# Kernel tuning notes

Hardware: AMD Instinct MI355X
Metric: run time of the kernel (lower is better)

The kernel has to match this reference:

```python
import jax, jax.numpy as jnp
import numpy as np

C = 256  # channels
B, H, W = 16, 64, 64


def _conv1x1(x, w, b):
    # x: [B,Cin,H,W], w: [Cout,Cin], b: [Cout] -> [B,Cout,H,W]
    return jnp.einsum('bchw,oc->bohw', x, w) + b[None, :, None, None]


def _axis_attn(x, wq, bq, wf, bf, axis):
    # axis: -1 for 'W', -2 for 'H'
    qkv = _conv1x1(x, wq, bq)                      # [B,1+2C,H,W]
    query = qkv[:, :1]                             # [B,1,H,W]
    key = qkv[:, 1:1 + C]                          # [B,C,H,W]
    value = qkv[:, 1 + C:]                         # [B,C,H,W]
    scores = jax.nn.softmax(query, axis=axis)      # softmax over spatial axis
    context = jnp.sum(key * scores, axis=axis, keepdims=True)  # [B,C,H,1] or [B,C,1,W]
    gate = jax.nn.sigmoid(value)
    out = x + gate * context                       # broadcast over reduced axis
    return _conv1x1(out, wf, bf)


def setup_inputs() -> dict:
    key = jax.random.key(0)
    ks = jax.random.split(key, 5)
    s_qkv = 1.0 / np.sqrt(C)
    s_fus = 1.0 / np.sqrt(C)
    return {
        'x': jax.random.normal(ks[0], (B, C, H, W), dtype=jnp.float32),
        'qkvW_w': jax.random.normal(ks[1], (1 + 2 * C, C), dtype=jnp.float32) * s_qkv,
        'qkvW_b': jnp.zeros((1 + 2 * C,), dtype=jnp.float32),
        'qkvH_w': jax.random.normal(ks[2], (1 + 2 * C, C), dtype=jnp.float32) * s_qkv,
        'qkvH_b': jnp.zeros((1 + 2 * C,), dtype=jnp.float32),
        'fusW_w': jax.random.normal(ks[3], (C, C), dtype=jnp.float32) * s_fus,
        'fusW_b': jnp.zeros((C,), dtype=jnp.float32),
        'fusH_w': jax.random.normal(ks[4], (C, C), dtype=jnp.float32) * s_fus,
        'fusH_b': jnp.zeros((C,), dtype=jnp.float32),
    }


def reference(x, qkvW_w, qkvW_b, qkvH_w, qkvH_b, fusW_w, fusW_b, fusH_w, fusH_b):
    x_w = _axis_attn(x, qkvW_w, qkvW_b, fusW_w, fusW_b, axis=-1)
    x_h = _axis_attn(x_w, qkvH_w, qkvH_b, fusH_w, fusH_b, axis=-2)
    return x_h
```

## Files before the change

kernel.cpp:

```cpp
#include <hip/hip_runtime.h>

typedef unsigned short u16;
typedef unsigned int u32;
typedef __attribute__((ext_vector_type(8))) short bf16x8;
typedef __attribute__((ext_vector_type(4))) float f32x4;

__device__ __forceinline__ u16 f2bf(float f) {
    u32 u = __builtin_bit_cast(u32, f);
    u += 0x7FFFu + ((u >> 16) & 1u);
    return (u16)(u >> 16);
}
__device__ __forceinline__ float bf2f(u16 s) {
    u32 u = ((u32)s) << 16;
    return __builtin_bit_cast(float, u);
}
__device__ __forceinline__ float sigm(float x) {
    return 1.0f / (1.0f + __expf(-x));
}
__device__ __forceinline__ void gload16(const u16* g, u16* l) {
    __builtin_amdgcn_global_load_lds(
        (const __attribute__((address_space(1))) void*)g,
        (__attribute__((address_space(3))) void*)l, 16, 0, 0);
}

__global__ __launch_bounds__(256) void transpose_in(const float* __restrict__ x,
                                                    u16* __restrict__ xp) {
    __shared__ float tile[64][65];
    int bid = blockIdx.x;
    int ct = bid & 3, h = (bid >> 2) & 63, b = bid >> 8;
    int t = threadIdx.x;
    int tr = t >> 4, tc = t & 15;
    const float* src = x + (((size_t)(b * 256 + ct * 64) * 64 + h) * 64);
#pragma unroll
    for (int i = 0; i < 4; ++i) {
        int c = tr + i * 16;
        float4 v = *(const float4*)(src + (size_t)c * 4096 + tc * 4);
        tile[c][tc * 4 + 0] = v.x;
        tile[c][tc * 4 + 1] = v.y;
        tile[c][tc * 4 + 2] = v.z;
        tile[c][tc * 4 + 3] = v.w;
    }
    __syncthreads();
    u16* dst = xp + ((size_t)((b * 64 + h) * 64)) * 256 + ct * 64;
#pragma unroll
    for (int i = 0; i < 4; ++i) {
        int w = tr + i * 16;
        ushort4 o;
        o.x = f2bf(tile[tc * 4 + 0][w]);
        o.y = f2bf(tile[tc * 4 + 1][w]);
        o.z = f2bf(tile[tc * 4 + 2][w]);
        o.w = f2bf(tile[tc * 4 + 3][w]);
        *(ushort4*)(dst + (size_t)w * 256 + tc * 4) = o;
    }
}

__global__ __launch_bounds__(256) void prep_w(const float* __restrict__ qw,
                                              const float* __restrict__ qb,
                                              const float* __restrict__ fw,
                                              const float* __restrict__ fb,
                                              float* __restrict__ wq0,
                                              u16* __restrict__ wkv,
                                              float* __restrict__ bkv,
                                              u16* __restrict__ wf,
                                              float* __restrict__ bff) {
    int i = blockIdx.x * 256 + threadIdx.x;
    if (i < 513 * 256) {
        int o = i >> 8, c = i & 255;
        float v = qw[i];
        if (o == 0) wq0[c] = v;
        else        wkv[(size_t)(o - 1) * 256 + c] = f2bf(v);
    }
    if (i < 65536) wf[i] = f2bf(fw[i]);
    if (i < 512)   bkv[i] = qb[i + 1];
    if (i < 256)   bff[i] = fb[i];
}

template <int AXIS>
__global__ __launch_bounds__(256) void line_ctx(
    const u16* __restrict__ A, const u16* __restrict__ Wk,
    const float* __restrict__ wq0, const float* __restrict__ bkv,
    float* __restrict__ ctx) {
    __shared__ alignas(16) u16 Xl[64 * 256];
    __shared__ float ql[64];
    __shared__ float sc[64];
    __shared__ alignas(16) float ys[256];
    int t = threadIdx.x, lane = t & 63, wv = t >> 6;
    int l = blockIdx.x;
    auto prow = [&](int r) -> size_t {
        if (AXIS == 0) return (size_t)l * 64 + r;
        else           return (size_t)(l >> 6) * 4096 + (size_t)r * 64 + (l & 63);
    };
#pragma unroll
    for (int i = 0; i < 8; ++i) {
        int row = i * 8 + wv * 2 + (lane >> 5);
        int slot = (lane & 31) ^ (row & 7);
        gload16(A + prow(row) * 256 + slot * 8, &Xl[(i * 8 + wv * 2) * 256]);
    }
    __syncthreads();
    {
        int row = t >> 2, g = t & 3;
        const float* wp = wq0 + g * 64;
        float a = 0.f;
#pragma unroll
        for (int cc = 0; cc < 8; ++cc) {
            int slot = (g * 8 + cc) ^ (row & 7);
            bf16x8 v = *(const bf16x8*)&Xl[row * 256 + slot * 8];
#pragma unroll
            for (int j = 0; j < 8; ++j) a += bf2f((u16)v[j]) * wp[cc * 8 + j];
        }
        a += __shfl_xor(a, 1);
        a += __shfl_xor(a, 2);
        if (g == 0) ql[row] = a;
    }
    __syncthreads();
    if (t < 64) {
        float qv = ql[t];
        float m = qv;
#pragma unroll
        for (int off = 32; off > 0; off >>= 1) m = fmaxf(m, __shfl_xor(m, off));
        float e = __expf(qv - m);
        float s = e;
#pragma unroll
        for (int off = 32; off > 0; off >>= 1) s += __shfl_xor(s, off);
        sc[t] = e / s;
    }
    __syncthreads();
    {
        int chunk = t >> 3, e7 = t & 7;
        float a = 0.f;
#pragma unroll 8
        for (int p = 0; p < 64; ++p) {
            int slot = chunk ^ (p & 7);
            a += bf2f(Xl[p * 256 + slot * 8 + e7]) * sc[p];
        }
        ys[t] = a;
    }
    __syncthreads();
    {
        const u16* wk = Wk + (size_t)t * 256;
        float a = 0.f;
#pragma unroll
        for (int kc = 0; kc < 32; ++kc) {
            bf16x8 w = *(const bf16x8*)(wk + kc * 8);
#pragma unroll
            for (int j = 0; j < 8; ++j) a += bf2f((u16)w[j]) * ys[kc * 8 + j];
        }
        ctx[(size_t)l * 256 + t] = a + bkv[t];
    }
}

template <int AXIS>
__global__ __launch_bounds__(256, 2) void val_gate(
    const u16* __restrict__ A, const u16* __restrict__ Wv,
    const float* __restrict__ bv, const float* __restrict__ ctx,
    u16* __restrict__ G) {
    int h = blockIdx.x;
    int xcd = h & 7, slot = h >> 3;
    int otile = slot & 1, ptile = xcd * 64 + (slot >> 1);
    __shared__ alignas(16) u16 Asm[128 * 64];
    __shared__ alignas(16) u16 Bsm[128 * 64];
    int p0 = ptile * 128, o0 = otile * 128;
    int t = threadIdx.x, lane = t & 63, wv = t >> 6;
    int wm = (wv >> 1) * 64, wn = (wv & 1) * 64;
    int l7 = lane & 7;
    int srcoff = (lane >> 3) * 256 + (((lane & 7) ^ (lane >> 3)) * 8);
    int arow = lane & 15, kgrp = lane >> 4;
    f32x4 zero = {0.f, 0.f, 0.f, 0.f};
    f32x4 acc[4][4];
#pragma unroll
    for (int i = 0; i < 4; ++i)
#pragma unroll
        for (int jj = 0; jj < 4; ++jj) acc[i][jj] = zero;

    for (int k0 = 0; k0 < 256; k0 += 64) {
        __syncthreads();
#pragma unroll
        for (int it = 0; it < 4; ++it) {
            int r0 = it * 32 + wv * 8;
            gload16(A + (size_t)(p0 + r0) * 256 + k0 + srcoff, &Asm[r0 * 64]);
            gload16(Wv + (size_t)(o0 + r0) * 256 + k0 + srcoff, &Bsm[r0 * 64]);
        }
        __syncthreads();
#pragma unroll
        for (int kk = 0; kk < 64; kk += 32) {
            int soff = (((kk >> 3) + kgrp) ^ l7) << 3;
            bf16x8 af[4], bfv[4];
#pragma unroll
            for (int mi = 0; mi < 4; ++mi)
                af[mi] = *(const bf16x8*)&Asm[(wm + mi * 16 + arow) * 64 + soff];
#pragma unroll
            for (int ni = 0; ni < 4; ++ni)
                bfv[ni] = *(const bf16x8*)&Bsm[(wn + ni * 16 + arow) * 64 + soff];
#pragma unroll
            for (int mi = 0; mi < 4; ++mi)
#pragma unroll
                for (int ni = 0; ni < 4; ++ni)
                    acc[mi][ni] = __builtin_amdgcn_mfma_f32_16x16x32_bf16(
                        af[mi], bfv[ni], acc[mi][ni], 0, 0, 0);
        }
    }
#pragma unroll
    for (int mi = 0; mi < 4; ++mi) {
#pragma unroll
        for (int ni = 0; ni < 4; ++ni) {
            int col = o0 + wn + ni * 16 + arow;
            float bias = bv[col];
#pragma unroll
            for (int r = 0; r < 4; ++r) {
                int row = p0 + wm + mi * 16 + (kgrp << 2) + r;
                int line = (AXIS == 0) ? (row >> 6) : ((row >> 12) * 64 + (row & 63));
                float cx = ctx[(size_t)line * 256 + col];
                float xv = bf2f(A[(size_t)row * 256 + col]);
                float v = acc[mi][ni][r] + bias;
                G[(size_t)row * 256 + col] = f2bf(xv + sigm(v) * cx);
            }
        }
    }
}

template <int MODE>
__global__ __launch_bounds__(256, 2) void gemm_k(
    const u16* __restrict__ A, const u16* __restrict__ Bw,
    const float* __restrict__ bias,
    u16* __restrict__ bOut, float* __restrict__ fOut) {
    int h = blockIdx.x;
    int xcd = h & 7, slot = h >> 3;
    int otile = slot & 1, ptile = xcd * 64 + (slot >> 1);
    __shared__ alignas(16) u16 Asm[128 * 64];
    __shared__ alignas(16) u16 Bsm[128 * 64];
    int p0 = ptile * 128, o0 = otile * 128;
    int t = threadIdx.x, lane = t & 63, wv = t >> 6;
    int wm = (wv >> 1) * 64, wn = (wv & 1) * 64;
    int l7 = lane & 7;
    int srcoff = (lane >> 3) * 256 + (((lane & 7) ^ (lane >> 3)) * 8);
    int arow = lane & 15, kgrp = lane >> 4;
    f32x4 zero = {0.f, 0.f, 0.f, 0.f};
    f32x4 acc[4][4];
#pragma unroll
    for (int i = 0; i < 4; ++i)
#pragma unroll
        for (int jj = 0; jj < 4; ++jj) acc[i][jj] = zero;

    for (int k0 = 0; k0 < 256; k0 += 64) {
        __syncthreads();
#pragma unroll
        for (int it = 0; it < 4; ++it) {
            int r0 = it * 32 + wv * 8;
            gload16(A + (size_t)(p0 + r0) * 256 + k0 + srcoff, &Asm[r0 * 64]);
            gload16(Bw + (size_t)(o0 + r0) * 256 + k0 + srcoff, &Bsm[r0 * 64]);
        }
        __syncthreads();
#pragma unroll
        for (int kk = 0; kk < 64; kk += 32) {
            int soff = (((kk >> 3) + kgrp) ^ l7) << 3;
            bf16x8 af[4], bfv[4];
#pragma unroll
            for (int mi = 0; mi < 4; ++mi)
                af[mi] = *(const bf16x8*)&Asm[(wm + mi * 16 + arow) * 64 + soff];
#pragma unroll
            for (int ni = 0; ni < 4; ++ni)
                bfv[ni] = *(const bf16x8*)&Bsm[(wn + ni * 16 + arow) * 64 + soff];
#pragma unroll
            for (int mi = 0; mi < 4; ++mi)
#pragma unroll
                for (int ni = 0; ni < 4; ++ni)
                    acc[mi][ni] = __builtin_amdgcn_mfma_f32_16x16x32_bf16(
                        af[mi], bfv[ni], acc[mi][ni], 0, 0, 0);
        }
    }
#pragma unroll
    for (int mi = 0; mi < 4; ++mi) {
#pragma unroll
        for (int ni = 0; ni < 4; ++ni) {
            int col = o0 + wn + ni * 16 + arow;
            float bv = bias[col];
#pragma unroll
            for (int r = 0; r < 4; ++r) {
                int row = p0 + wm + mi * 16 + ((lane >> 4) << 2) + r;
                float v = acc[mi][ni][r] + bv;
                if (MODE == 1) {
                    bOut[(size_t)row * 256 + col] = f2bf(v);
                } else {
                    fOut[((size_t)((row >> 12) * 256 + col)) * 4096 + (row & 4095)] = v;
                }
            }
        }
    }
}

extern "C" void kernel_launch(void* const* d_in, const int* in_sizes, int n_in,
                              void* d_out, int out_size, void* d_ws, size_t ws_size,
                              hipStream_t stream) {
    const float* x   = (const float*)d_in[0];
    const float* qWw = (const float*)d_in[1];
    const float* qWb = (const float*)d_in[2];
    const float* qHw = (const float*)d_in[3];
    const float* qHb = (const float*)d_in[4];
    const float* fWw = (const float*)d_in[5];
    const float* fWb = (const float*)d_in[6];
    const float* fHw = (const float*)d_in[7];
    const float* fHb = (const float*)d_in[8];
    float* out = (float*)d_out;

    char* ws = (char*)d_ws;
    size_t off = 0;
    auto carve = [&](size_t bytes) -> void* {
        off = (off + 255) & ~(size_t)255;
        void* p = ws + off;
        off += bytes;
        return p;
    };
    const size_t P = 65536;
    u16*   xp  = (u16*)carve(P * 256 * 2);
    u16*   kb  = (u16*)carve(P * 256 * 2);
    u16*   vb  = (u16*)carve(P * 256 * 2);
    float* ctxb = (float*)carve(1024 * 256 * 4);
    float* wq01 = (float*)carve(256 * 4);
    u16*   wkv1 = (u16*)carve(512 * 256 * 2);
    float* bkv1 = (float*)carve(512 * 4);
    u16*   wf1  = (u16*)carve(65536 * 2);
    float* bf1  = (float*)carve(256 * 4);
    float* wq02 = (float*)carve(256 * 4);
    u16*   wkv2 = (u16*)carve(512 * 256 * 2);
    float* bkv2 = (float*)carve(512 * 4);
    u16*   wf2  = (u16*)carve(65536 * 2);
    float* bf2  = (float*)carve(256 * 4);

    prep_w<<<513, 256, 0, stream>>>(qWw, qWb, fWw, fWb, wq01, wkv1, bkv1, wf1, bf1);
    prep_w<<<513, 256, 0, stream>>>(qHw, qHb, fHw, fHb, wq02, wkv2, bkv2, wf2, bf2);
    transpose_in<<<4096, 256, 0, stream>>>(x, xp);

    line_ctx<0><<<1024, 256, 0, stream>>>(xp, wkv1, wq01, bkv1, ctxb);
    val_gate<0><<<1024, 256, 0, stream>>>(xp, wkv1 + 256 * 256, bkv1 + 256,
                                          ctxb, kb);
    gemm_k<1><<<1024, 256, 0, stream>>>(kb, wf1, bf1, vb, nullptr);
    line_ctx<1><<<1024, 256, 0, stream>>>(vb, wkv2, wq02, bkv2, ctxb);
    val_gate<1><<<1024, 256, 0, stream>>>(vb, wkv2 + 256 * 256, bkv2 + 256,
                                          ctxb, kb);
    gemm_k<2><<<1024, 256, 0, stream>>>(kb, wf2, bf2, nullptr, out);
    (void)in_sizes; (void)n_in; (void)out_size; (void)ws_size;
}
```

Before: 167.3 us.

## Vectorize GEMM epilogues via operand swap, LDS transpose, and shared ctx tiles

Measured after the change: 178.4 us. 6.6% more time.

```diff
diff --git a/kernel.cpp b/kernel.cpp
--- a/kernel.cpp
+++ b/kernel.cpp
@@ -159,12 +159,21 @@
     int otile = slot & 1, ptile = xcd * 64 + (slot >> 1);
     __shared__ alignas(16) u16 Asm[128 * 64];
     __shared__ alignas(16) u16 Bsm[128 * 64];
-    int p0 = ptile * 128, o0 = otile * 128;
+    __shared__ alignas(16) float ctxs[2][128];
+    int o0 = otile * 128;
     int t = threadIdx.x, lane = t & 63, wv = t >> 6;
-    int wm = (wv >> 1) * 64, wn = (wv & 1) * 64;
-    int l7 = lane & 7;
-    int srcoff = (lane >> 3) * 256 + (((lane & 7) ^ (lane >> 3)) * 8);
-    int arow = lane & 15, kgrp = lane >> 4;
+    int arow = lane & 15, kgrp = lane >> 4, l7 = lane & 7;
+    int rowhalf = wv & 1, chhalf = wv >> 1;
+    auto prow = [&](int r) -> size_t {
+        if (AXIS == 0) return (size_t)ptile * 128 + r;
+        else           return (size_t)(ptile >> 5) * 4096 + (size_t)(r & 63) * 64 +
+                              ((ptile & 31) * 2) + (r >> 6);
+    };
+    int lbase = (AXIS == 0) ? (ptile * 2) : ((ptile >> 5) * 64 + (ptile & 31) * 2);
+    {
+        int ll = t >> 7, cl = t & 127;
+        ctxs[ll][cl] = ctx[(size_t)(lbase + ll) * 256 + o0 + cl];
+    }
     f32x4 zero = {0.f, 0.f, 0.f, 0.f};
     f32x4 acc[4][4];
 #pragma unroll
@@ -177,43 +186,47 @@
 #pragma unroll
         for (int it = 0; it < 4; ++it) {
             int r0 = it * 32 + wv * 8;
-            gload16(A + (size_t)(p0 + r0) * 256 + k0 + srcoff, &Asm[r0 * 64]);
-            gload16(Wv + (size_t)(o0 + r0) * 256 + k0 + srcoff, &Bsm[r0 * 64]);
+            int rr = r0 + (lane >> 3);
+            int chs = ((l7 ^ (lane >> 3)) * 8);
+            gload16(A + prow(rr) * 256 + k0 + chs, &Asm[r0 * 64]);
+            gload16(Wv + (size_t)(o0 + rr) * 256 + k0 + chs, &Bsm[r0 * 64]);
         }
         __syncthreads();
 #pragma unroll
         for (int kk = 0; kk < 64; kk += 32) {
             int soff = (((kk >> 3) + kgrp) ^ l7) << 3;
-            bf16x8 af[4], bfv[4];
-#pragma unroll
-            for (int mi = 0; mi < 4; ++mi)
-                af[mi] = *(const bf16x8*)&Asm[(wm + mi * 16 + arow) * 64 + soff];
-#pragma unroll
-            for (int ni = 0; ni < 4; ++ni)
-                bfv[ni] = *(const bf16x8*)&Bsm[(wn + ni * 16 + arow) * 64 + soff];
-#pragma unroll
-            for (int mi = 0; mi < 4; ++mi)
-#pragma unroll
-                for (int ni = 0; ni < 4; ++ni)
-                    acc[mi][ni] = __builtin_amdgcn_mfma_f32_16x16x32_bf16(
-                        af[mi], bfv[ni], acc[mi][ni], 0, 0, 0);
-        }
-    }
-#pragma unroll
-    for (int mi = 0; mi < 4; ++mi) {
-#pragma unroll
-        for (int ni = 0; ni < 4; ++ni) {
-            int col = o0 + wn + ni * 16 + arow;
-            float bias = bv[col];
-#pragma unroll
-            for (int r = 0; r < 4; ++r) {
-                int row = p0 + wm + mi * 16 + (kgrp << 2) + r;
-                int line = (AXIS == 0) ? (row >> 6) : ((row >> 12) * 64 + (row & 63));
-                float cx = ctx[(size_t)line * 256 + col];
-                float xv = bf2f(A[(size_t)row * 256 + col]);
-                float v = acc[mi][ni][r] + bias;
-                G[(size_t)row * 256 + col] = f2bf(xv + sigm(v) * cx);
-            }
+            bf16x8 xf[4], wf[4];
+#pragma unroll
+            for (int xi = 0; xi < 4; ++xi)
+                xf[xi] = *(const bf16x8*)&Asm[(rowhalf * 64 + xi * 16 + arow) * 64 + soff];
+#pragma unroll
+            for (int wi = 0; wi < 4; ++wi)
+                wf[wi] = *(const bf16x8*)&Bsm[(chhalf * 64 + wi * 16 + arow) * 64 + soff];
+#pragma unroll
+            for (int wi = 0; wi < 4; ++wi)
+#pragma unroll
+                for (int xi = 0; xi < 4; ++xi)
+                    acc[wi][xi] = __builtin_amdgcn_mfma_f32_16x16x32_bf16(
+                        wf[wi], xf[xi], acc[wi][xi], 0, 0, 0);
+        }
+    }
+#pragma unroll
+    for (int wi = 0; wi < 4; ++wi) {
+        int chl = chhalf * 64 + wi * 16 + kgrp * 4;
+        int ch = o0 + chl;
+        f32x4 bq = *(const f32x4*)&bv[ch];
+        f32x4 cx = *(const f32x4*)&ctxs[rowhalf][chl];
+#pragma unroll
+        for (int xi = 0; xi < 4; ++xi) {
+            int row = rowhalf * 64 + xi * 16 + arow;
+            size_t p = prow(row);
+            ushort4 xv = *(const ushort4*)(A + p * 256 + ch);
+            ushort4 o;
+            o.x = f2bf(bf2f(xv.x) + sigm(acc[wi][xi][0] + bq[0]) * cx[0]);
+            o.y = f2bf(bf2f(xv.y) + sigm(acc[wi][xi][1] + bq[1]) * cx[1]);
+            o.z = f2bf(bf2f(xv.z) + sigm(acc[wi][xi][2] + bq[2]) * cx[2]);
+            o.w = f2bf(bf2f(xv.w) + sigm(acc[wi][xi][3] + bq[3]) * cx[3]);
+            *(ushort4*)(G + p * 256 + ch) = o;
         }
     }
 }
@@ -228,6 +241,7 @@
     int otile = slot & 1, ptile = xcd * 64 + (slot >> 1);
     __shared__ alignas(16) u16 Asm[128 * 64];
     __shared__ alignas(16) u16 Bsm[128 * 64];
+    __shared__ alignas(16) float tb[(MODE == 2) ? 64 * 132 : 4];
     int p0 = ptile * 128, o0 = otile * 128;
     int t = threadIdx.x, lane = t & 63, wv = t >> 6;
     int wm = (wv >> 1) * 64, wn = (wv & 1) * 64;
@@ -260,30 +274,69 @@
 #pragma unroll
             for (int ni = 0; ni < 4; ++ni)
                 bfv[ni] = *(const bf16x8*)&Bsm[(wn + ni * 16 + arow) * 64 + soff];
-#pragma unroll
-            for (int mi = 0; mi < 4; ++mi)
+            if (MODE == 1) {
 #pragma unroll
                 for (int ni = 0; ni < 4; ++ni)
-                    acc[mi][ni] = __builtin_amdgcn_mfma_f32_16x16x32_bf16(
-                        af[mi], bfv[ni], acc[mi][ni], 0, 0, 0);
-        }
-    }
-#pragma unroll
-    for (int mi = 0; mi < 4; ++mi) {
+#pragma unroll
+                    for (int mi = 0; mi < 4; ++mi)
+                        acc[ni][mi] = __builtin_amdgcn_mfma_f32_16x16x32_bf16(
+                            bfv[ni], af[mi], acc[ni][mi], 0, 0, 0);
+            } else {
+#pragma unroll
+                for (int mi = 0; mi < 4; ++mi)
+#pragma unroll
+                    for (int ni = 0; ni < 4; ++ni)
+                        acc[mi][ni] = __builtin_amdgcn_mfma_f32_16x16x32_bf16(
+                            af[mi], bfv[ni], acc[mi][ni], 0, 0, 0);
+            }
+        }
+    }
+    if (MODE == 1) {
 #pragma unroll
         for (int ni = 0; ni < 4; ++ni) {
-            int col = o0 + wn + ni * 16 + arow;
-            float bv = bias[col];
-#pragma unroll
-            for (int r = 0; r < 4; ++r) {
-                int row = p0 + wm + mi * 16 + ((lane >> 4) << 2) + r;
-                float v = acc[mi][ni][r] + bv;
-                if (MODE == 1) {
-                    bOut[(size_t)row * 256 + col] = f2bf(v);
-                } else {
-                    fOut[((size_t)((row >> 12) * 256 + col)) * 4096 + (row & 4095)] = v;
+            int col0 = o0 + wn + ni * 16 + kgrp * 4;
+            f32x4 bq = *(const f32x4*)&bias[col0];
+#pragma unroll
+            for (int mi = 0; mi < 4; ++mi) {
+                int row = p0 + wm + mi * 16 + arow;
+                ushort4 o;
+                o.x = f2bf(acc[ni][mi][0] + bq[0]);
+                o.y = f2bf(acc[ni][mi][1] + bq[1]);
+                o.z = f2bf(acc[ni][mi][2] + bq[2]);
+                o.w = f2bf(acc[ni][mi][3] + bq[3]);
+                *(ushort4*)(bOut + (size_t)row * 256 + col0) = o;
+            }
+        }
+    } else {
+        int bb = p0 >> 12, pl = p0 & 4095;
+#pragma unroll
+        for (int cp = 0; cp < 2; ++cp) {
+            if ((wv & 1) == cp) {
+#pragma unroll
+                for (int ni = 0; ni < 4; ++ni) {
+                    int c = ni * 16 + arow;
+                    float bvv = bias[o0 + cp * 64 + c];
+#pragma unroll
+                    for (int mi = 0; mi < 4; ++mi) {
+                        int r0w = wm + mi * 16 + kgrp * 4;
+                        f32x4 v;
+                        v[0] = acc[mi][ni][0] + bvv;
+                        v[1] = acc[mi][ni][1] + bvv;
+                        v[2] = acc[mi][ni][2] + bvv;
+                        v[3] = acc[mi][ni][3] + bvv;
+                        *(f32x4*)&tb[c * 132 + r0w] = v;
+                    }
                 }
             }
+            __syncthreads();
+#pragma unroll
+            for (int i = 0; i < 8; ++i) {
+                int c = i * 8 + (t >> 5);
+                f32x4 v = *(const f32x4*)&tb[c * 132 + (t & 31) * 4];
+                *(float4*)&fOut[(size_t)(bb * 256 + o0 + cp * 64 + c) * 4096 +
+                                pl + (t & 31) * 4] = *(float4*)&v;
+            }
+            if (cp == 0) __syncthreads();
         }
     }
 }
```

## Fuse value-gate GEMM with fusion GEMM keeping gated tile in LDS

Applied to the files above, without the earlier changes.

Result: slower. 189.8 us (+13.5%).

```diff
diff --git a/kernel.cpp b/kernel.cpp
--- a/kernel.cpp
+++ b/kernel.cpp
@@ -59,20 +59,25 @@
                                               const float* __restrict__ fw,
                                               const float* __restrict__ fb,
                                               float* __restrict__ wq0,
-                                              u16* __restrict__ wkv,
+                                              u16* __restrict__ wkvK,
+                                              u16* __restrict__ wkvV,
                                               float* __restrict__ bkv,
-                                              u16* __restrict__ wf,
+                                              u16* __restrict__ wfP,
                                               float* __restrict__ bff) {
     int i = blockIdx.x * 256 + threadIdx.x;
     if (i < 513 * 256) {
         int o = i >> 8, c = i & 255;
         float v = qw[i];
-        if (o == 0) wq0[c] = v;
-        else        wkv[(size_t)(o - 1) * 256 + c] = f2bf(v);
-    }
-    if (i < 65536) wf[i] = f2bf(fw[i]);
-    if (i < 512)   bkv[i] = qb[i + 1];
-    if (i < 256)   bff[i] = fb[i];
+        if (o == 0)        wq0[c] = v;
+        else if (o < 257)  wkvK[(size_t)(o - 1) * 256 + c] = f2bf(v);
+        else               wkvV[(c >> 3) * 2048 + (o - 257) * 8 + (c & 7)] = f2bf(v);
+    }
+    if (i < 65536) {
+        int o = i >> 8, c = i & 255;
+        wfP[(c >> 3) * 2048 + o * 8 + (c & 7)] = f2bf(fw[i]);
+    }
+    if (i < 512) bkv[i] = qb[i + 1];
+    if (i < 256) bff[i] = fb[i];
 }
 
 template <int AXIS>
@@ -149,140 +154,144 @@
     }
 }
 
-template <int AXIS>
-__global__ __launch_bounds__(256, 2) void val_gate(
-    const u16* __restrict__ A, const u16* __restrict__ Wv,
-    const float* __restrict__ bv, const float* __restrict__ ctx,
-    u16* __restrict__ G) {
-    int h = blockIdx.x;
-    int xcd = h & 7, slot = h >> 3;
-    int otile = slot & 1, ptile = xcd * 64 + (slot >> 1);
-    __shared__ alignas(16) u16 Asm[128 * 64];
-    __shared__ alignas(16) u16 Bsm[128 * 64];
-    int p0 = ptile * 128, o0 = otile * 128;
-    int t = threadIdx.x, lane = t & 63, wv = t >> 6;
-    int wm = (wv >> 1) * 64, wn = (wv & 1) * 64;
-    int l7 = lane & 7;
-    int srcoff = (lane >> 3) * 256 + (((lane & 7) ^ (lane >> 3)) * 8);
+template <int AXIS, int MODE>
+__global__ __launch_bounds__(512, 2) void fused_stage(
+    const u16* __restrict__ A, const u16* __restrict__ WvP,
+    const float* __restrict__ bv, const u16* __restrict__ WfP,
+    const float* __restrict__ bfb, const float* __restrict__ ctx,
+    u16* __restrict__ bOut, float* __restrict__ fOut) {
+    __shared__ alignas(16) u16 Xsm[128 * 256];
+    __shared__ alignas(16) u16 Wsm[1024 * 8];
+    int t = threadIdx.x, lane = t & 63;
+    int wv = t >> 6, rowhalf = wv >> 2, chslab = (wv & 3) * 64;
     int arow = lane & 15, kgrp = lane >> 4;
+    int p0 = blockIdx.x * 128;
+#pragma unroll
+    for (int i = 0; i < 8; ++i) {
+        int d = t + i * 512;
+        int row = d >> 5, chunk = d & 31;
+        gload16(A + (size_t)(p0 + row) * 256 + ((chunk ^ (row & 7)) * 8),
+                &Xsm[d * 8]);
+    }
     f32x4 zero = {0.f, 0.f, 0.f, 0.f};
     f32x4 acc[4][4];
 #pragma unroll
-    for (int i = 0; i < 4; ++i)
-#pragma unroll
-        for (int jj = 0; jj < 4; ++jj) acc[i][jj] = zero;
-
-    for (int k0 = 0; k0 < 256; k0 += 64) {
+    for (int a = 0; a < 4; ++a)
+#pragma unroll
+        for (int b = 0; b < 4; ++b) acc[a][b] = zero;
+    for (int k0 = 0; k0 < 256; k0 += 32) {
         __syncthreads();
-#pragma unroll
-        for (int it = 0; it < 4; ++it) {
-            int r0 = it * 32 + wv * 8;
-            gload16(A + (size_t)(p0 + r0) * 256 + k0 + srcoff, &Asm[r0 * 64]);
-            gload16(Wv + (size_t)(o0 + r0) * 256 + k0 + srcoff, &Bsm[r0 * 64]);
-        }
+        gload16(WvP + k0 * 256 + t * 8, &Wsm[t * 8]);
+        gload16(WvP + k0 * 256 + (t + 512) * 8, &Wsm[(t + 512) * 8]);
         __syncthreads();
-#pragma unroll
-        for (int kk = 0; kk < 64; kk += 32) {
-            int soff = (((kk >> 3) + kgrp) ^ l7) << 3;
-            bf16x8 af[4], bfv[4];
-#pragma unroll
-            for (int mi = 0; mi < 4; ++mi)
-                af[mi] = *(const bf16x8*)&Asm[(wm + mi * 16 + arow) * 64 + soff];
-#pragma unroll
-            for (int ni = 0; ni < 4; ++ni)
-                bfv[ni] = *(const bf16x8*)&Bsm[(wn + ni * 16 + arow) * 64 + soff];
-#pragma unroll
-            for (int mi = 0; mi < 4; ++mi)
-#pragma unroll
-                for (int ni = 0; ni < 4; ++ni)
-                    acc[mi][ni] = __builtin_amdgcn_mfma_f32_16x16x32_bf16(
-                        af[mi], bfv[ni], acc[mi][ni], 0, 0, 0);
-        }
-    }
-#pragma unroll
-    for (int mi = 0; mi < 4; ++mi) {
-#pragma unroll
-        for (int ni = 0; ni < 4; ++ni) {
-            int col = o0 + wn + ni * 16 + arow;
-            float bias = bv[col];
-#pragma unroll
-            for (int r = 0; r < 4; ++r) {
-                int row = p0 + wm + mi * 16 + (kgrp << 2) + r;
-                int line = (AXIS == 0) ? (row >> 6) : ((row >> 12) * 64 + (row & 63));
-                float cx = ctx[(size_t)line * 256 + col];
-                float xv = bf2f(A[(size_t)row * 256 + col]);
-                float v = acc[mi][ni][r] + bias;
-                G[(size_t)row * 256 + col] = f2bf(xv + sigm(v) * cx);
+        bf16x8 wf[4], xf[4];
+#pragma unroll
+        for (int wi = 0; wi < 4; ++wi)
+            wf[wi] = *(const bf16x8*)&Wsm[kgrp * 2048 + (chslab + wi * 16 + arow) * 8];
+#pragma unroll
+        for (int xi = 0; xi < 4; ++xi) {
+            int p = rowhalf * 64 + xi * 16 + arow;
+            xf[xi] = *(const bf16x8*)&Xsm[p * 256 + (((k0 >> 3) + kgrp) ^ (p & 7)) * 8];
+        }
+#pragma unroll
+        for (int wi = 0; wi < 4; ++wi)
+#pragma unroll
+            for (int xi = 0; xi < 4; ++xi)
+                acc[wi][xi] = __builtin_amdgcn_mfma_f32_16x16x32_bf16(
+                    wf[wi], xf[xi], acc[wi][xi], 0, 0, 0);
+    }
+    __syncthreads();
+#pragma unroll
+    for (int wi = 0; wi < 4; ++wi) {
+        int ch = chslab + wi * 16 + kgrp * 4;
+        f32x4 bq = *(const f32x4*)&bv[ch];
+        f32x4 cx0;
+        if (AXIS == 0)
+            cx0 = *(const f32x4*)&ctx[(size_t)((p0 >> 6) + rowhalf) * 256 + ch];
+#pragma unroll
+        for (int xi = 0; xi < 4; ++xi) {
+            int row = rowhalf * 64 + xi * 16 + arow;
+            f32x4 cx;
+            if (AXIS == 0) {
+                cx = cx0;
+            } else {
+                int pg = p0 + row;
+                int line = ((pg >> 12) << 6) + (pg & 63);
+                cx = *(const f32x4*)&ctx[(size_t)line * 256 + ch];
             }
-        }
-    }
-}
-
-template <int MODE>
-__global__ __launch_bounds__(256, 2) void gemm_k(
-    const u16* __restrict__ A, const u16* __restrict__ Bw,
-    const float* __restrict__ bias,
-    u16* __restrict__ bOut, float* __restrict__ fOut) {
-    int h = blockIdx.x;
-    int xcd = h & 7, slot = h >> 3;
-    int otile = slot & 1, ptile = xcd * 64 + (slot >> 1);
-    __shared__ alignas(16) u16 Asm[128 * 64];
-    __shared__ alignas(16) u16 Bsm[128 * 64];
-    int p0 = ptile * 128, o0 = otile * 128;
-    int t = threadIdx.x, lane = t & 63, wv = t >> 6;
-    int wm = (wv >> 1) * 64, wn = (wv & 1) * 64;
-    int l7 = lane & 7;
-    int srcoff = (lane >> 3) * 256 + (((lane & 7) ^ (lane >> 3)) * 8);
-    int arow = lane & 15, kgrp = lane >> 4;
-    f32x4 zero = {0.f, 0.f, 0.f, 0.f};
-    f32x4 acc[4][4];
-#pragma unroll
-    for (int i = 0; i < 4; ++i)
-#pragma unroll
-        for (int jj = 0; jj < 4; ++jj) acc[i][jj] = zero;
-
-    for (int k0 = 0; k0 < 256; k0 += 64) {
+            int idx = row * 256 + (((ch >> 3) ^ (row & 7)) * 8) + (ch & 7);
+            ushort4 xv = *(const ushort4*)&Xsm[idx];
+            ushort4 o;
+            o.x = f2bf(bf2f(xv.x) + sigm(acc[wi][xi][0] + bq[0]) * cx[0]);
+            o.y = f2bf(bf2f(xv.y) + sigm(acc[wi][xi][1] + bq[1]) * cx[1]);
+            o.z = f2bf(bf2f(xv.z) + sigm(acc[wi][xi][2] + bq[2]) * cx[2]);
+            o.w = f2bf(bf2f(xv.w) + sigm(acc[wi][xi][3] + bq[3]) * cx[3]);
+            *(ushort4*)&Xsm[idx] = o;
+        }
+    }
+#pragma unroll
+    for (int a = 0; a < 4; ++a)
+#pragma unroll
+        for (int b = 0; b < 4; ++b) acc[a][b] = zero;
+    for (int k0 = 0; k0 < 256; k0 += 32) {
         __syncthreads();
-#pragma unroll
-        for (int it = 0; it < 4; ++it) {
-            int r0 = it * 32 + wv * 8;
-            gload16(A + (size_t)(p0 + r0) * 256 + k0 + srcoff, &Asm[r0 * 64]);
-            gload16(Bw + (size_t)(o0 + r0) * 256 + k0 + srcoff, &Bsm[r0 * 64]);
-        }
+        gload16(WfP + k0 * 256 + t * 8, &Wsm[t * 8]);
+        gload16(WfP + k0 * 256 + (t + 512) * 8, &Wsm[(t + 512) * 8]);
         __syncthreads();
-#pragma unroll
-        for (int kk = 0; kk < 64; kk += 32) {
-            int soff = (((kk >> 3) + kgrp) ^ l7) << 3;
-            bf16x8 af[4], bfv[4];
-#pragma unroll
-            for (int mi = 0; mi < 4; ++mi)
-                af[mi] = *(const bf16x8*)&Asm[(wm + mi * 16 + arow) * 64 + soff];
-#pragma unroll
-            for (int ni = 0; ni < 4; ++ni)
-                bfv[ni] = *(const bf16x8*)&Bsm[(wn + ni * 16 + arow) * 64 + soff];
-#pragma unroll
-            for (int mi = 0; mi < 4; ++mi)
-#pragma unroll
-                for (int ni = 0; ni < 4; ++ni)
-                    acc[mi][ni] = __builtin_amdgcn_mfma_f32_16x16x32_bf16(
-                        af[mi], bfv[ni], acc[mi][ni], 0, 0, 0);
-        }
-    }
-#pragma unroll
-    for (int mi = 0; mi < 4; ++mi) {
-#pragma unroll
-        for (int ni = 0; ni < 4; ++ni) {
-            int col = o0 + wn + ni * 16 + arow;
-            float bv = bias[col];
-#pragma unroll
-            for (int r = 0; r < 4; ++r) {
-                int row = p0 + wm + mi * 16 + ((lane >> 4) << 2) + r;
-                float v = acc[mi][ni][r] + bv;
-                if (MODE == 1) {
-                    bOut[(size_t)row * 256 + col] = f2bf(v);
-                } else {
-                    fOut[((size_t)((row >> 12) * 256 + col)) * 4096 + (row & 4095)] = v;
-                }
+        bf16x8 wf[4], gf[4];
+#pragma unroll
+        for (int wi = 0; wi < 4; ++wi)
+            wf[wi] = *(const bf16x8*)&Wsm[kgrp * 2048 + (chslab + wi * 16 + arow) * 8];
+#pragma unroll
+        for (int xi = 0; xi < 4; ++xi) {
+            int p = rowhalf * 64 + xi * 16 + arow;
+            gf[xi] = *(const bf16x8*)&Xsm[p * 256 + (((k0 >> 3) + kgrp) ^ (p & 7)) * 8];
+        }
+        if (MODE == 1) {
+#pragma unroll
+            for (int wi = 0; wi < 4; ++wi)
+#pragma unroll
+                for (int xi = 0; xi < 4; ++xi)
+                    acc[wi][xi] = __builtin_amdgcn_mfma_f32_16x16x32_bf16(
+                        wf[wi], gf[xi], acc[wi][xi], 0, 0, 0);
+        } else {
+#pragma unroll
+            for (int xi = 0; xi < 4; ++xi)
+#pragma unroll
+                for (int wi = 0; wi < 4; ++wi)
+                    acc[xi][wi] = __builtin_amdgcn_mfma_f32_16x16x32_bf16(
+                        gf[xi], wf[wi], acc[xi][wi], 0, 0, 0);
+        }
+    }
+    if (MODE == 1) {
+#pragma unroll
+        for (int wi = 0; wi < 4; ++wi) {
+            int ch = chslab + wi * 16 + kgrp * 4;
+            f32x4 bq = *(const f32x4*)&bfb[ch];
+#pragma unroll
+            for (int xi = 0; xi < 4; ++xi) {
+                int row = rowhalf * 64 + xi * 16 + arow;
+                ushort4 o;
+                o.x = f2bf(acc[wi][xi][0] + bq[0]);
+                o.y = f2bf(acc[wi][xi][1] + bq[1]);
+                o.z = f2bf(acc[wi][xi][2] + bq[2]);
+                o.w = f2bf(acc[wi][xi][3] + bq[3]);
+                *(ushort4*)(bOut + (size_t)(p0 + row) * 256 + ch) = o;
+            }
+        }
+    } else {
+        int bb = p0 >> 12;
+#pragma unroll
+        for (int mi = 0; mi < 4; ++mi) {
+            int row0 = rowhalf * 64 + mi * 16 + kgrp * 4;
+#pragma unroll
+            for (int ni = 0; ni < 4; ++ni) {
+                int ch = chslab + ni * 16 + arow;
+                float bc = bfb[ch];
+                f32x4 v = acc[mi][ni];
+                v[0] += bc; v[1] += bc; v[2] += bc; v[3] += bc;
+                *(f32x4*)&fOut[((size_t)(bb * 256 + ch)) * 4096 +
+                               ((p0 + row0) & 4095)] = v;
             }
         }
     }
@@ -311,32 +320,33 @@
         return p;
     };
     const size_t P = 65536;
-    u16*   xp  = (u16*)carve(P * 256 * 2);
-    u16*   kb  = (u16*)carve(P * 256 * 2);
-    u16*   vb  = (u16*)carve(P * 256 * 2);
+    u16*   xp   = (u16*)carve(P * 256 * 2);
+    u16*   vb   = (u16*)carve(P * 256 * 2);
     float* ctxb = (float*)carve(1024 * 256 * 4);
-    float* wq01 = (float*)carve(256 * 4);
-    u16*   wkv1 = (u16*)carve(512 * 256 * 2);
-    float* bkv1 = (float*)carve(512 * 4);
-    u16*   wf1  = (u16*)carve(65536 * 2);
-    float* bf1  = (float*)carve(256 * 4);
-    float* wq02 = (float*)carve(256 * 4);
-    u16*   wkv2 = (u16*)carve(512 * 256 * 2);
-    float* bkv2 = (float*)carve(512 * 4);
-    u16*   wf2  = (u16*)carve(65536 * 2);
-    float* bf2  = (float*)carve(256 * 4);
-
-    prep_w<<<513, 256, 0, stream>>>(qWw, qWb, fWw, fWb, wq01, wkv1, bkv1, wf1, bf1);
-    prep_w<<<513, 256, 0, stream>>>(qHw, qHb, fHw, fHb, wq02, wkv2, bkv2, wf2, bf2);
+    float* wq01  = (float*)carve(256 * 4);
+    u16*   wkvK1 = (u16*)carve(256 * 256 * 2);
+    u16*   wkvV1 = (u16*)carve(256 * 256 * 2);
+    float* bkv1  = (float*)carve(512 * 4);
+    u16*   wfP1  = (u16*)carve(65536 * 2);
+    float* bff1  = (float*)carve(256 * 4);
+    float* wq02  = (float*)carve(256 * 4);
+    u16*   wkvK2 = (u16*)carve(256 * 256 * 2);
+    u16*   wkvV2 = (u16*)carve(256 * 256 * 2);
+    float* bkv2  = (float*)carve(512 * 4);
+    u16*   wfP2  = (u16*)carve(65536 * 2);
+    float* bff2  = (float*)carve(256 * 4);
+
+    prep_w<<<513, 256, 0, stream>>>(qWw, qWb, fWw, fWb, wq01, wkvK1, wkvV1,
+                                    bkv1, wfP1, bff1);
+    prep_w<<<513, 256, 0, stream>>>(qHw, qHb, fHw, fHb, wq02, wkvK2, wkvV2,
+                                    bkv2, wfP2, bff2);
     transpose_in<<<4096, 256, 0, stream>>>(x, xp);
 
-    line_ctx<0><<<1024, 256, 0, stream>>>(xp, wkv1, wq01, bkv1, ctxb);
-    val_gate<0><<<1024, 256, 0, stream>>>(xp, wkv1 + 256 * 256, bkv1 + 256,
-                                          ctxb, kb);
-    gemm_k<1><<<1024, 256, 0, stream>>>(kb, wf1, bf1, vb, nullptr);
-    line_ctx<1><<<1024, 256, 0, stream>>>(vb, wkv2, wq02, bkv2, ctxb);
-    val_gate<1><<<1024, 256, 0, stream>>>(vb, wkv2 + 256 * 256, bkv2 + 256,
-                                          ctxb, kb);
-    gemm_k<2><<<1024, 256, 0, stream>>>(kb, wf2, bf2, nullptr, out);
+    line_ctx<0><<<1024, 256, 0, stream>>>(xp, wkvK1, wq01, bkv1, ctxb);
+    fused_stage<0, 1><<<512, 512, 0, stream>>>(xp, wkvV1, bkv1 + 256, wfP1,
+                                               bff1, ctxb, vb, nullptr);
+    line_ctx<1><<<1024, 256, 0, stream>>>(vb, wkvK2, wq02, bkv2, ctxb);
+    fused_stage<1, 2><<<512, 512, 0, stream>>>(vb, wkvV2, bkv2 + 256, wfP2,
+                                               bff2, ctxb, nullptr, out);
     (void)in_sizes; (void)n_in; (void)out_size; (void)ws_size;
 }
```
